# Kernel optimization log

Hardware: AMD Instinct MI355X
Metric: run time of the kernel (lower is better)

## Reference

```python
import jax, jax.numpy as jnp
import numpy as np


def _bilinear(x, py, px):
    # x: [B,C,H,W]; py,px: [B,K,Ho,Wo] fractional sample coords (zero pad outside)
    B, C, H, W = x.shape
    K, Ho, Wo = py.shape[1], py.shape[2], py.shape[3]
    xf = x.reshape(B, C, H * W)
    y0 = jnp.floor(py)
    x0 = jnp.floor(px)

    def gather(yi, xi):
        valid = (yi >= 0) & (yi <= H - 1) & (xi >= 0) & (xi <= W - 1)
        yc = jnp.clip(yi, 0, H - 1).astype(jnp.int32)
        xc = jnp.clip(xi, 0, W - 1).astype(jnp.int32)
        idx = (yc * W + xc).reshape(B, 1, -1)  # [B,1,K*Ho*Wo]
        v = jnp.take_along_axis(xf, idx, axis=2)  # [B,C,K*Ho*Wo]
        return v * valid.reshape(B, 1, -1)

    wy1 = (py - y0).reshape(B, 1, -1)
    wx1 = (px - x0).reshape(B, 1, -1)
    wy0 = 1.0 - wy1
    wx0 = 1.0 - wx1
    v = (gather(y0, x0) * (wy0 * wx0)
         + gather(y0, x0 + 1) * (wy0 * wx1)
         + gather(y0 + 1, x0) * (wy1 * wx0)
         + gather(y0 + 1, x0 + 1) * (wy1 * wx1))
    return v.reshape(B, C, K, Ho, Wo)


def _deform_merge(x, w_off, b_off, w_def, gamma, beta):
    B, C, H, W = x.shape
    Co = w_def.shape[0]
    K, stride = 4, 2  # 2x2 kernel
    Ho, Wo = H // 2, W // 2
    # offset-predicting conv (same k/s/p as deform conv): [B, 2K, Ho, Wo]
    off = jax.lax.conv_general_dilated(x, w_off, (stride, stride), 'VALID')
    off = off + b_off[None, :, None, None]
    off = off.reshape(B, K, 2, Ho, Wo)  # (dy, dx) per kernel tap
    ky = jnp.arange(K) // 2
    kx = jnp.arange(K) % 2
    base_y = (jnp.arange(Ho) * stride)[None, None, :, None] + ky[None, :, None, None]
    base_x = (jnp.arange(Wo) * stride)[None, None, None, :] + kx[None, :, None, None]
    py = base_y.astype(x.dtype) + off[:, :, 0]
    px = base_x.astype(x.dtype) + off[:, :, 1]
    sampled = _bilinear(x, py, px)  # [B,C,K,Ho,Wo]
    y = jnp.einsum('bckhw,ock->bohw', sampled, w_def.reshape(Co, C, K))
    # BatchNorm2d (training-mode batch stats, eps=1e-5) + exact GELU
    mu = y.mean(axis=(0, 2, 3), keepdims=True)
    var = y.var(axis=(0, 2, 3), keepdims=True)
    yn = (y - mu) * jax.lax.rsqrt(var + 1e-5)
    yn = yn * gamma[None, :, None, None] + beta[None, :, None, None]
    yg = jax.nn.gelu(yn, approximate=False)
    return yg.reshape(B, Co, Ho * Wo).transpose(0, 2, 1)  # [B, L/4, Co]


def setup_inputs() -> dict:
    key = jax.random.key(0)
    k0, k1, k2 = jax.random.split(key, 3)
    B, C, H, W, Co = 16, 96, 112, 112, 192
    x = jax.random.normal(k0, (B, C, H, W), jnp.float32)
    # conv_offset: 2*kh*kw = 8 output channels (zero-init in mmcv; small random here)
    w_off = jax.random.normal(k1, (8, C, 2, 2), jnp.float32) * 0.01
    b_off = jnp.zeros((8,), jnp.float32)
    w_def = jax.random.normal(k2, (Co, C, 2, 2), jnp.float32) * (1.0 / np.sqrt(C * 4))
    gamma = jnp.ones((Co,), jnp.float32)
    beta = jnp.zeros((Co,), jnp.float32)
    return {"x": x, "h": H, "w": W, "w_off": w_off, "b_off": b_off,
            "w_def": w_def, "gamma": gamma, "beta": beta}


def reference(x, h, w, w_off, b_off, w_def, gamma, beta):
    assert x.shape[2] == h and x.shape[3] == w
    return _deform_merge(x, w_off, b_off, w_def, gamma, beta)
```

## Files before the change

### kernel.cpp

```cpp
#include <hip/hip_runtime.h>
#include <math.h>

#define BB 16
#define CC 96
#define HH 112
#define WW 112
#define HO 56
#define WO 56
#define LL (HO*WO)
#define CO 192
#define CKD 384
#define NPIX (BB*LL)

#define TPX 28
#define CHK 8
#define NCHUNK 12
#define WROWS 4
#define WCOLS 64
#define WSTRIDE 260
#define APAD 40

#define WS_SSUM  16
#define WS_SSQS  208
#define WS_B_OFF 4096
#define B_ELEMS  73728

typedef short bf16x8 __attribute__((ext_vector_type(8)));
typedef float f32x4  __attribute__((ext_vector_type(4)));

__device__ __forceinline__ void split8(const float4 a0, const float4 a1,
                                       bf16x8& hi, bf16x8& lo)
{
    float f[8] = {a0.x, a0.y, a0.z, a0.w, a1.x, a1.y, a1.z, a1.w};
    #pragma unroll
    for (int j = 0; j < 8; ++j) {
        unsigned bits = __float_as_uint(f[j]);
        float fh = __uint_as_float(bits & 0xFFFF0000u);
        float fl = f[j] - fh;
        hi[j] = (short)(bits >> 16);
        lo[j] = (short)(__float_as_uint(fl) >> 16);
    }
}

__global__ void k_zero(float* __restrict__ ws) {
    int t = threadIdx.x;
    if (t < 384) ws[WS_SSUM + t] = 0.f;
}

__global__ void k_prep(const float* __restrict__ w_def,
                       unsigned short* __restrict__ bhi,
                       unsigned short* __restrict__ blo,
                       float* __restrict__ ws)
{
    if (blockIdx.x == 0 && threadIdx.x < 384) ws[WS_SSUM + threadIdx.x] = 0.f;
    int t = blockIdx.x * 256 + threadIdx.x;
    if (t >= 12 * 12 * 64) return;
    int ln  = t & 63;
    int ks  = (t >> 6) % 12;
    int ntg = t / (64 * 12);
    int n  = ntg * 16 + (ln & 15);
    int k0 = ks * 32 + (ln >> 4) * 8;
    const float* wp = w_def + (size_t)n * CKD + k0;
    #pragma unroll
    for (int j = 0; j < 8; ++j) {
        float f = wp[j];
        unsigned bits = __float_as_uint(f);
        float fh = __uint_as_float(bits & 0xFFFF0000u);
        float fl = f - fh;
        bhi[t * 8 + j] = (unsigned short)(bits >> 16);
        blo[t * 8 + j] = (unsigned short)(__float_as_uint(fl) >> 16);
    }
}

template<bool PREP>
__global__ __launch_bounds__(256, 4) void k_main(
    const float* __restrict__ x,
    const float* __restrict__ w_off,
    const float* __restrict__ b_off,
    const float* __restrict__ w_def,
    const unsigned short* __restrict__ bhi,
    const unsigned short* __restrict__ blo,
    float* __restrict__ yout,
    float* __restrict__ ws)
{
    __shared__ float win[CHK * WSTRIDE];
    __shared__ unsigned short smAh[32 * APAD];
    __shared__ unsigned short smAl[32 * APAD];
    __shared__ float soff[TPX * 8];

    const int tid = threadIdx.x;
    const int b  = blockIdx.y;
    const int bx = blockIdx.x;
    const int oy  = bx >> 1;
    const int ox0 = (bx & 1) * TPX;
    const int iy  = oy * 2;
    const int ix0 = ox0 * 2;
    const int ln = tid & 63;
    const int w  = tid >> 6;

    float dacc = 0.f;
    const int cpix = tid >> 3;
    const int coch = tid & 7;
    const int spair = tid / 14;
    const int sq    = tid % 14;
    for (int ch = 0; ch < NCHUNK; ++ch) {
        __syncthreads();
        if (tid < 224) {
            int c = spair >> 1, r = spair & 1;
            const float* src = x + (((size_t)(b * CC + ch * CHK + c) * HH) + iy + r) * WW + ix0 + sq * 4;
            *(float4*)&win[(c * 2 + r) * 56 + sq * 4] = *(const float4*)src;
        }
        __syncthreads();
        if (tid < 224) {
            const float* wb = w_off + (size_t)coch * (CC * 4) + ch * CHK * 4;
            #pragma unroll
            for (int c = 0; c < CHK; ++c) {
                float2 t0 = *(const float2*)&win[(c * 2 + 0) * 56 + 2 * cpix];
                float2 t1 = *(const float2*)&win[(c * 2 + 1) * 56 + 2 * cpix];
                float4 a = *(const float4*)(wb + c * 4);
                dacc += t0.x * a.x + t0.y * a.y + t1.x * a.z + t1.y * a.w;
            }
        }
    }
    if (tid < 224) soff[cpix * 8 + coch] = dacc + b_off[coch];
    if (tid < 128) {
        int rr = 28 + (tid >> 5), cc = tid & 31;
        smAh[rr * APAD + cc] = 0;
        smAl[rr * APAD + cc] = 0;
    }

    const int row0 = ln & 15;
    const int kg   = ln >> 4;
    const int skk = tid & 31;
    const int sc  = skk >> 2;
    const int sk  = skk & 3;
    const int sky = sk >> 1, skx = sk & 1;
    const int wr0 = iy - 1, wc0 = ix0 - 4;

    f32x4 acc[2][3];
    #pragma unroll
    for (int mt = 0; mt < 2; ++mt)
        #pragma unroll
        for (int nt = 0; nt < 3; ++nt)
            acc[mt][nt] = (f32x4){0.f, 0.f, 0.f, 0.f};

    for (int ch = NCHUNK - 1; ch >= 0; --ch) {
        __syncthreads();
        #pragma unroll
        for (int j = 0; j < 2; ++j) {
            int li = tid + 256 * j;
            int cg = li & 15;
            int pr = li >> 4;
            int r = pr & 3, c = pr >> 2;
            int gr = min(max(wr0 + r, 0), HH - 1);
            int gc0 = wc0 + cg * 4;
            const float* src = x + (((size_t)(b * CC + ch * CHK + c) * HH) + gr) * WW;
            float4 v;
            if (gc0 >= 0 && gc0 <= WW - 4) {
                v = *(const float4*)(src + gc0);
            } else {
                v.x = src[min(max(gc0 + 0, 0), WW - 1)];
                v.y = src[min(max(gc0 + 1, 0), WW - 1)];
                v.z = src[min(max(gc0 + 2, 0), WW - 1)];
                v.w = src[min(max(gc0 + 3, 0), WW - 1)];
            }
            *(float4*)&win[c * WSTRIDE + r * WCOLS + cg * 4] = v;
        }
        __syncthreads();
        {
            const float* xc = x + ((size_t)(b * CC + ch * CHK + sc) * HH) * WW;
            const float* wchan = &win[sc * WSTRIDE];
            #pragma unroll
            for (int j = 0; j < 4; ++j) {
                if (j < 3 || tid < 128) {
                    int pix = (tid >> 5) + 8 * j;
                    float2 so = *(const float2*)&soff[pix * 8 + 2 * sk];
                    float fy = (float)(iy + sky) + so.x;
                    float fx = (float)(ix0 + 2 * pix + skx) + so.y;
                    float y0f = floorf(fy), x0f = floorf(fx);
                    int y0 = (int)y0f, x0 = (int)x0f;
                    float wy1 = fy - y0f, wx1 = fx - x0f;
                    float wy0 = 1.f - wy1, wx0 = 1.f - wx1;
                    int y1 = y0 + 1, x1 = x0 + 1;
                    bool vy0 = (y0 >= 0) && (y0 <= HH - 1);
                    bool vy1 = (y1 >= 0) && (y1 <= HH - 1);
                    bool vx0 = (x0 >= 0) && (x0 <= WW - 1);
                    bool vx1 = (x1 >= 0) && (x1 <= WW - 1);
                    int cy0 = min(max(y0, 0), HH - 1), cy1 = min(max(y1, 0), HH - 1);
                    int cx0 = min(max(x0, 0), WW - 1), cx1 = min(max(x1, 0), WW - 1);
                    float w00 = (vy0 && vx0) ? wy0 * wx0 : 0.f;
                    float w01 = (vy0 && vx1) ? wy0 * wx1 : 0.f;
                    float w10 = (vy1 && vx0) ? wy1 * wx0 : 0.f;
                    float w11 = (vy1 && vx1) ? wy1 * wx1 : 0.f;
                    int ry0 = cy0 - wr0, ry1 = cy1 - wr0;
                    int rx0 = cx0 - wc0, rx1 = cx1 - wc0;
                    bool inw = ((unsigned)ry0 <= (unsigned)(WROWS - 1)) &&
                               ((unsigned)ry1 <= (unsigned)(WROWS - 1)) &&
                               ((unsigned)rx0 <= (unsigned)(WCOLS - 1)) &&
                               ((unsigned)rx1 <= (unsigned)(WCOLS - 1));
                    float v;
                    if (inw) {
                        v = w00 * wchan[ry0 * WCOLS + rx0] + w01 * wchan[ry0 * WCOLS + rx1]
                          + w10 * wchan[ry1 * WCOLS + rx0] + w11 * wchan[ry1 * WCOLS + rx1];
                    } else {
                        v = w00 * xc[cy0 * WW + cx0] + w01 * xc[cy0 * WW + cx1]
                          + w10 * xc[cy1 * WW + cx0] + w11 * xc[cy1 * WW + cx1];
                    }
                    unsigned u = __float_as_uint(v);
                    float fh = __uint_as_float(u & 0xFFFF0000u);
                    smAh[pix * APAD + skk] = (unsigned short)(u >> 16);
                    smAl[pix * APAD + skk] = (unsigned short)(__float_as_uint(v - fh) >> 16);
                }
            }
        }
        __syncthreads();
        bf16x8 ah[2], al[2];
        #pragma unroll
        for (int mt = 0; mt < 2; ++mt) {
            ah[mt] = *(const bf16x8*)&smAh[(mt * 16 + row0) * APAD + kg * 8];
            al[mt] = *(const bf16x8*)&smAl[(mt * 16 + row0) * APAD + kg * 8];
        }
        #pragma unroll
        for (int nt = 0; nt < 3; ++nt) {
            bf16x8 bh, bl;
            if (PREP) {
                size_t idx = ((size_t)(((w * 3 + nt) * 12 + ch) * 64) + ln) * 8;
                bh = *(const bf16x8*)(bhi + idx);
                bl = *(const bf16x8*)(blo + idx);
            } else {
                const float* wp = w_def + (size_t)(w * 48 + nt * 16 + row0) * CKD
                                + ch * 32 + kg * 8;
                float4 b0 = *(const float4*)wp;
                float4 b1 = *(const float4*)(wp + 4);
                split8(b0, b1, bh, bl);
            }
            #pragma unroll
            for (int mt = 0; mt < 2; ++mt) {
                acc[mt][nt] = __builtin_amdgcn_mfma_f32_16x16x32_bf16(ah[mt], bh, acc[mt][nt], 0, 0, 0);
                acc[mt][nt] = __builtin_amdgcn_mfma_f32_16x16x32_bf16(ah[mt], bl, acc[mt][nt], 0, 0, 0);
                acc[mt][nt] = __builtin_amdgcn_mfma_f32_16x16x32_bf16(al[mt], bh, acc[mt][nt], 0, 0, 0);
            }
        }
    }

    #pragma unroll
    for (int nt = 0; nt < 3; ++nt) {
        float s = 0.f, q = 0.f;
        #pragma unroll
        for (int mt = 0; mt < 2; ++mt)
            #pragma unroll
            for (int r = 0; r < 4; ++r) {
                float v = acc[mt][nt][r];
                s += v; q += v * v;
            }
        s += __shfl_xor(s, 16); s += __shfl_xor(s, 32);
        q += __shfl_xor(q, 16); q += __shfl_xor(q, 32);
        if (ln < 16) {
            atomicAdd(&ws[WS_SSUM + w * 48 + nt * 16 + ln], s);
            atomicAdd(&ws[WS_SSQS + w * 48 + nt * 16 + ln], q);
        }
    }
    size_t obase = (size_t)b * LL + (size_t)oy * WO + ox0;
    #pragma unroll
    for (int mt = 0; mt < 2; ++mt)
        #pragma unroll
        for (int r = 0; r < 4; ++r) {
            int pp = mt * 16 + kg * 4 + r;
            if (pp < TPX) {
                float* dst = yout + (obase + pp) * CO + w * 48 + row0;
                dst[0]  = acc[mt][0][r];
                dst[16] = acc[mt][1][r];
                dst[32] = acc[mt][2][r];
            }
        }
}

__global__ __launch_bounds__(256) void k_bn_gelu(
    float* __restrict__ out,
    const float* __restrict__ gamma,
    const float* __restrict__ beta,
    const float* __restrict__ ws)
{
    __shared__ float ssc[CO], ssh[CO];
    int t = threadIdx.x;
    if (t < CO) {
        float n = (float)NPIX;
        float mu = ws[WS_SSUM + t] / n;
        float var = ws[WS_SSQS + t] / n - mu * mu;
        float sc = gamma[t] * rsqrtf(fmaxf(var, 0.f) + 1e-5f);
        ssc[t] = sc;
        ssh[t] = beta[t] - mu * sc;
    }
    __syncthreads();
    long long i4 = ((long long)blockIdx.x * 256 + t) * 4;
    if (i4 >= (long long)NPIX * CO) return;
    int o0 = (int)(i4 % CO);
    float4* p = (float4*)(out + i4);
    float4 v = *p;
    float f[4] = { v.x, v.y, v.z, v.w };
    #pragma unroll
    for (int j = 0; j < 4; ++j) {
        float z = ssc[o0 + j] * f[j] + ssh[o0 + j];
        f[j] = 0.5f * z * (1.f + erff(z * 0.70710678118654752f));
    }
    v.x = f[0]; v.y = f[1]; v.z = f[2]; v.w = f[3];
    *p = v;
}

extern "C" void kernel_launch(void* const* d_in, const int* in_sizes, int n_in,
                              void* d_out, int out_size, void* d_ws, size_t ws_size,
                              hipStream_t stream)
{
    const float *x = nullptr, *w_off = nullptr, *b_off = nullptr;
    const float *w_def = nullptr, *gamma = nullptr, *beta = nullptr;
    for (int i = 0; i < n_in; ++i) {
        int s = in_sizes[i];
        if      (s == 19267584) x     = (const float*)d_in[i];
        else if (s == 3072)     w_off = (const float*)d_in[i];
        else if (s == 8)        b_off = (const float*)d_in[i];
        else if (s == 73728)    w_def = (const float*)d_in[i];
        else if (s == 192) { if (!gamma) gamma = (const float*)d_in[i];
                             else        beta  = (const float*)d_in[i]; }
    }
    if (!x || !w_off || !b_off || !w_def || !gamma || !beta) {
        x = (const float*)d_in[0]; w_off = (const float*)d_in[3];
        b_off = (const float*)d_in[4]; w_def = (const float*)d_in[5];
        gamma = (const float*)d_in[6]; beta = (const float*)d_in[7];
    }

    float* ws = (float*)d_ws;
    float* out = (float*)d_out;

    unsigned short* bhi = (unsigned short*)((char*)d_ws + WS_B_OFF);
    unsigned short* blo = bhi + B_ELEMS;
    bool prep = ws_size >= (size_t)(WS_B_OFF + 2 * B_ELEMS * sizeof(unsigned short));

    if (prep) {
        k_prep<<<36, 256, 0, stream>>>(w_def, bhi, blo, ws);
        k_main<true><<<dim3(112, BB), 256, 0, stream>>>(x, w_off, b_off, w_def, bhi, blo, out, ws);
    } else {
        k_zero<<<1, 384, 0, stream>>>(ws);
        k_main<false><<<dim3(112, BB), 256, 0, stream>>>(x, w_off, b_off, w_def, bhi, blo, out, ws);
    }
    k_bn_gelu<<<dim3((int)(((long long)NPIX*CO/4 + 255) / 256)), 256, 0, stream>>>(out, gamma, beta, ws);
}
```

Measured before the change: 308.2 us.

## Fuse main GEMM and BN+GELU via cooperative grid sync with register-held tiles

Replaces the separate main kernel and BN/GELU pass with a cooperative kernel. Each block processes two tiles and keeps their accumulators in registers, then does a grid-wide sync after the atomic statistics and writes normalized GELU output directly. This removes the round trip of writing the pre-norm output to global memory and reading it back, plus one kernel launch. In exchange it raises register pressure with doubled accumulators, requires all 896 blocks to be co-resident, and adds grid-sync cost. If the cooperative launch fails it falls back to the old path.

Result: slower. 667.1 us (+116.5%).

```diff
diff --git a/kernel.cpp b/kernel.cpp
--- a/kernel.cpp
+++ b/kernel.cpp
@@ -1,5 +1,8 @@
 #include <hip/hip_runtime.h>
+#include <hip/hip_cooperative_groups.h>
 #include <math.h>
+
+namespace cg = cooperative_groups;
 
 #define BB 16
 #define CC 96
@@ -73,24 +76,13 @@
 }
 
 template<bool PREP>
-__global__ __launch_bounds__(256, 4) void k_main(
-    const float* __restrict__ x,
-    const float* __restrict__ w_off,
-    const float* __restrict__ b_off,
-    const float* __restrict__ w_def,
-    const unsigned short* __restrict__ bhi,
-    const unsigned short* __restrict__ blo,
-    float* __restrict__ yout,
-    float* __restrict__ ws)
-{
-    __shared__ float win[CHK * WSTRIDE];
-    __shared__ unsigned short smAh[32 * APAD];
-    __shared__ unsigned short smAl[32 * APAD];
-    __shared__ float soff[TPX * 8];
-
-    const int tid = threadIdx.x;
-    const int b  = blockIdx.y;
-    const int bx = blockIdx.x;
+__device__ __forceinline__ void tile_body(
+    const float* __restrict__ x, const float* __restrict__ w_off,
+    const float* __restrict__ b_off, const float* __restrict__ w_def,
+    const unsigned short* __restrict__ bhi, const unsigned short* __restrict__ blo,
+    float* win, unsigned short* smAh, unsigned short* smAl, float* soff,
+    int b, int bx, int tid, f32x4 (*acc)[3])
+{
     const int oy  = bx >> 1;
     const int ox0 = (bx & 1) * TPX;
     const int iy  = oy * 2;
@@ -123,11 +115,6 @@
         }
     }
     if (tid < 224) soff[cpix * 8 + coch] = dacc + b_off[coch];
-    if (tid < 128) {
-        int rr = 28 + (tid >> 5), cc = tid & 31;
-        smAh[rr * APAD + cc] = 0;
-        smAl[rr * APAD + cc] = 0;
-    }
 
     const int row0 = ln & 15;
     const int kg   = ln >> 4;
@@ -136,13 +123,6 @@
     const int sk  = skk & 3;
     const int sky = sk >> 1, skx = sk & 1;
     const int wr0 = iy - 1, wc0 = ix0 - 4;
-
-    f32x4 acc[2][3];
-    #pragma unroll
-    for (int mt = 0; mt < 2; ++mt)
-        #pragma unroll
-        for (int nt = 0; nt < 3; ++nt)
-            acc[mt][nt] = (f32x4){0.f, 0.f, 0.f, 0.f};
 
     for (int ch = NCHUNK - 1; ch >= 0; --ch) {
         __syncthreads();
@@ -242,17 +222,62 @@
             }
         }
     }
+}
+
+template<bool PREP>
+__global__ __launch_bounds__(256, 4) void k_fused(
+    const float* __restrict__ x, const float* __restrict__ w_off,
+    const float* __restrict__ b_off, const float* __restrict__ w_def,
+    const unsigned short* __restrict__ bhi, const unsigned short* __restrict__ blo,
+    float* __restrict__ out, float* __restrict__ ws,
+    const float* __restrict__ gamma, const float* __restrict__ beta)
+{
+    __shared__ float win[CHK * WSTRIDE];
+    __shared__ unsigned short smAh[32 * APAD];
+    __shared__ unsigned short smAl[32 * APAD];
+    __shared__ float soff[TPX * 8];
+
+    const int tid = threadIdx.x;
+    const int b   = blockIdx.y;
+    const int ln = tid & 63;
+    const int w  = tid >> 6;
+    const int row0 = ln & 15;
+    const int kg   = ln >> 4;
+
+    if (tid < 128) {
+        int rr = 28 + (tid >> 5), cc = tid & 31;
+        smAh[rr * APAD + cc] = 0;
+        smAl[rr * APAD + cc] = 0;
+    }
+
+    f32x4 acc2[2][2][3];
+    #pragma unroll
+    for (int t = 0; t < 2; ++t)
+        #pragma unroll
+        for (int mt = 0; mt < 2; ++mt)
+            #pragma unroll
+            for (int nt = 0; nt < 3; ++nt)
+                acc2[t][mt][nt] = (f32x4){0.f, 0.f, 0.f, 0.f};
+
+    #pragma unroll 1
+    for (int t = 0; t < 2; ++t) {
+        int bx = blockIdx.x * 2 + t;
+        tile_body<PREP>(x, w_off, b_off, w_def, bhi, blo,
+                        win, smAh, smAl, soff, b, bx, tid, acc2[t]);
+    }
 
     #pragma unroll
     for (int nt = 0; nt < 3; ++nt) {
         float s = 0.f, q = 0.f;
         #pragma unroll
-        for (int mt = 0; mt < 2; ++mt)
-            #pragma unroll
-            for (int r = 0; r < 4; ++r) {
-                float v = acc[mt][nt][r];
-                s += v; q += v * v;
-            }
+        for (int t = 0; t < 2; ++t)
+            #pragma unroll
+            for (int mt = 0; mt < 2; ++mt)
+                #pragma unroll
+                for (int r = 0; r < 4; ++r) {
+                    float v = acc2[t][mt][nt][r];
+                    s += v; q += v * v;
+                }
         s += __shfl_xor(s, 16); s += __shfl_xor(s, 32);
         q += __shfl_xor(q, 16); q += __shfl_xor(q, 32);
         if (ln < 16) {
@@ -260,6 +285,98 @@
             atomicAdd(&ws[WS_SSQS + w * 48 + nt * 16 + ln], q);
         }
     }
+
+    __threadfence();
+    cg::this_grid().sync();
+
+    float scs[3], shs[3];
+    const float n = (float)NPIX;
+    #pragma unroll
+    for (int nt = 0; nt < 3; ++nt) {
+        int o = w * 48 + nt * 16 + row0;
+        float mu  = ws[WS_SSUM + o] / n;
+        float var = ws[WS_SSQS + o] / n - mu * mu;
+        float sc = gamma[o] * rsqrtf(fmaxf(var, 0.f) + 1e-5f);
+        scs[nt] = sc;
+        shs[nt] = beta[o] - mu * sc;
+    }
+
+    #pragma unroll
+    for (int t = 0; t < 2; ++t) {
+        int bx = blockIdx.x * 2 + t;
+        int oy = bx >> 1, ox0 = (bx & 1) * TPX;
+        size_t obase = (size_t)b * LL + (size_t)oy * WO + ox0;
+        #pragma unroll
+        for (int mt = 0; mt < 2; ++mt)
+            #pragma unroll
+            for (int r = 0; r < 4; ++r) {
+                int pp = mt * 16 + kg * 4 + r;
+                if (pp < TPX) {
+                    float* dst = out + (obase + pp) * CO + w * 48 + row0;
+                    #pragma unroll
+                    for (int nt = 0; nt < 3; ++nt) {
+                        float z = scs[nt] * acc2[t][mt][nt][r] + shs[nt];
+                        dst[nt * 16] = 0.5f * z * (1.f + erff(z * 0.70710678118654752f));
+                    }
+                }
+            }
+    }
+}
+
+template<bool PREP>
+__global__ __launch_bounds__(256, 4) void k_main(
+    const float* __restrict__ x, const float* __restrict__ w_off,
+    const float* __restrict__ b_off, const float* __restrict__ w_def,
+    const unsigned short* __restrict__ bhi, const unsigned short* __restrict__ blo,
+    float* __restrict__ yout, float* __restrict__ ws)
+{
+    __shared__ float win[CHK * WSTRIDE];
+    __shared__ unsigned short smAh[32 * APAD];
+    __shared__ unsigned short smAl[32 * APAD];
+    __shared__ float soff[TPX * 8];
+
+    const int tid = threadIdx.x;
+    const int b  = blockIdx.y;
+    const int bx = blockIdx.x;
+    const int ln = tid & 63;
+    const int w  = tid >> 6;
+    const int row0 = ln & 15;
+    const int kg   = ln >> 4;
+
+    if (tid < 128) {
+        int rr = 28 + (tid >> 5), cc = tid & 31;
+        smAh[rr * APAD + cc] = 0;
+        smAl[rr * APAD + cc] = 0;
+    }
+
+    f32x4 acc[2][3];
+    #pragma unroll
+    for (int mt = 0; mt < 2; ++mt)
+        #pragma unroll
+        for (int nt = 0; nt < 3; ++nt)
+            acc[mt][nt] = (f32x4){0.f, 0.f, 0.f, 0.f};
+
+    tile_body<PREP>(x, w_off, b_off, w_def, bhi, blo,
+                    win, smAh, smAl, soff, b, bx, tid, acc);
+
+    #pragma unroll
+    for (int nt = 0; nt < 3; ++nt) {
+        float s = 0.f, q = 0.f;
+        #pragma unroll
+        for (int mt = 0; mt < 2; ++mt)
+            #pragma unroll
+            for (int r = 0; r < 4; ++r) {
+                float v = acc[mt][nt][r];
+                s += v; q += v * v;
+            }
+        s += __shfl_xor(s, 16); s += __shfl_xor(s, 32);
+        q += __shfl_xor(q, 16); q += __shfl_xor(q, 32);
+        if (ln < 16) {
+            atomicAdd(&ws[WS_SSUM + w * 48 + nt * 16 + ln], s);
+            atomicAdd(&ws[WS_SSQS + w * 48 + nt * 16 + ln], q);
+        }
+    }
+    int oy = bx >> 1, ox0 = (bx & 1) * TPX;
     size_t obase = (size_t)b * LL + (size_t)oy * WO + ox0;
     #pragma unroll
     for (int mt = 0; mt < 2; ++mt)
@@ -335,12 +452,25 @@
     unsigned short* blo = bhi + B_ELEMS;
     bool prep = ws_size >= (size_t)(WS_B_OFF + 2 * B_ELEMS * sizeof(unsigned short));
 
-    if (prep) {
-        k_prep<<<36, 256, 0, stream>>>(w_def, bhi, blo, ws);
-        k_main<true><<<dim3(112, BB), 256, 0, stream>>>(x, w_off, b_off, w_def, bhi, blo, out, ws);
-    } else {
-        k_zero<<<1, 384, 0, stream>>>(ws);
-        k_main<false><<<dim3(112, BB), 256, 0, stream>>>(x, w_off, b_off, w_def, bhi, blo, out, ws);
-    }
-    k_bn_gelu<<<dim3((int)(((long long)NPIX*CO/4 + 255) / 256)), 256, 0, stream>>>(out, gamma, beta, ws);
-}
+    if (prep) k_prep<<<36, 256, 0, stream>>>(w_def, bhi, blo, ws);
+    else      k_zero<<<1, 384, 0, stream>>>(ws);
+
+    void* args[] = { (void*)&x, (void*)&w_off, (void*)&b_off, (void*)&w_def,
+                     (void*)&bhi, (void*)&blo, (void*)&out, (void*)&ws,
+                     (void*)&gamma, (void*)&beta };
+    hipError_t e;
+    if (prep)
+        e = hipLaunchCooperativeKernel(k_fused<true>,  dim3(56, BB), dim3(256),
+                                       args, 0, stream);
+    else
+        e = hipLaunchCooperativeKernel(k_fused<false>, dim3(56, BB), dim3(256),
+                                       args, 0, stream);
+
+    if (e != hipSuccess) {
+        if (prep)
+            k_main<true><<<dim3(112, BB), 256, 0, stream>>>(x, w_off, b_off, w_def, bhi, blo, out, ws);
+        else
+            k_main<false><<<dim3(112, BB), 256, 0, stream>>>(x, w_off, b_off, w_def, bhi, blo, out, ws);
+        k_bn_gelu<<<dim3((int)(((long long)NPIX*CO/4 + 255) / 256)), 256, 0, stream>>>(out, gamma, beta, ws);
+    }
+}
```
